# Kernel tuning notes

Hardware: AMD Instinct MI355X
Metric: run time of the kernel (lower is better)

## Reference

```python
import jax, jax.numpy as jnp
import numpy as np

B, N, C = 2, 2048, 1152
H = 16
HD = C // H  # 72
SCALE = HD ** -0.5
NEG = -100000000.0  # -1e8 bias for fp32 masked positions


def setup_inputs() -> dict:
    key = jax.random.key(0)
    k1, k2, k3, k4, k5 = jax.random.split(key, 5)
    x = jax.random.normal(k1, (B, N, C), dtype=jnp.float32)
    attn_mask = jax.random.randint(k2, (B, N), 0, 2, dtype=jnp.int32)
    w_qkv = jax.random.normal(k3, (3 * C, C), dtype=jnp.float32) * 0.02
    w_proj = jax.random.normal(k4, (C, C), dtype=jnp.float32) * 0.02
    b_proj = jax.random.normal(k5, (C,), dtype=jnp.float32) * 0.02
    return {"x": x, "attn_mask": attn_mask, "w_qkv": w_qkv, "w_proj": w_proj, "b_proj": b_proj}


def reference(x, attn_mask, w_qkv, w_proj, b_proj):
    # qkv projection: [B,N,3C] -> [3,B,H,N,HD]
    qkv = (x @ w_qkv.T).reshape(B, N, 3, H, HD).transpose(2, 0, 3, 1, 4)
    q, k, v = qkv[0], qkv[1], qkv[2]

    # additive mask bias from outer product of per-token 0/1 mask
    m = attn_mask.astype(x.dtype)          # [B,N]
    mm = m[:, :, None] * m[:, None, :]      # [B,N,N]
    bias = jnp.where(mm == 0, NEG, jnp.where(mm == 1, 0.0, mm))
    bias = bias[:, None, :, :]              # [B,1,N,N] broadcast over heads

    # math-branch attention: full QK^T, bias add, softmax, NaN patch, AV
    attn = jnp.einsum('bhqd,bhkd->bhqk', q, k) * SCALE + bias
    attn = jax.nn.softmax(attn, axis=-1)
    attn = jnp.where(jnp.isnan(attn), 0.0, attn)
    out = jnp.einsum('bhqk,bhkd->bqhd', attn, v).reshape(B, N, C)

    return out @ w_proj.T + b_proj
```

## Files before the change

kernel.cpp:

```cpp
#include <hip/hip_runtime.h>

#define B_   2
#define N_   2048
#define C_   1152
#define H_   16
#define HD_  72
#define QKV_W 3456
#define SCALE_ 0.11785113019775793f
#define NEG_  -100000000.0f
#define HDP  96
#define HDV  80
#define PRE_  0.1700219068852255f
#define FMAX_ 4.0f
#define KNEG_ 16384.0f

typedef _Float16  f16x8  __attribute__((ext_vector_type(8)));
typedef _Float16  f16x4  __attribute__((ext_vector_type(4)));
typedef float     f32x4  __attribute__((ext_vector_type(4)));

#define GLOAD_LDS16(gp, lp)                                                    \
  __builtin_amdgcn_global_load_lds(                                            \
      (const __attribute__((address_space(1))) void*)(gp),                     \
      (__attribute__((address_space(3))) void*)(lp), 16, 0, 0)

static __device__ __forceinline__ unsigned pack2h(_Float16 a, _Float16 b) {
  union { _Float16 h[2]; unsigned u; } u;
  u.h[0] = a; u.h[1] = b; return u.u;
}
typedef __fp16 fp16v2_builtin __attribute__((ext_vector_type(2)));
static __device__ __forceinline__ unsigned pkrtz(float a, float b) {
  union { fp16v2_builtin h; unsigned u; } u;
  u.h = __builtin_amdgcn_cvt_pkrtz(a, b);
  return u.u;
}

__global__ __launch_bounds__(256)
void split3_f16(const float* __restrict__ x, const float* __restrict__ wq,
                const float* __restrict__ wp,
                _Float16* __restrict__ xf, _Float16* __restrict__ wqf,
                _Float16* __restrict__ wpf,
                _Float16* __restrict__ Qf, _Float16* __restrict__ Kf,
                _Float16* __restrict__ Vt, const int* __restrict__ mask,
                float* __restrict__ meanAcc, int nmv,
                int n8x, int n8q, int n8p) {
  int i = blockIdx.x * 256 + threadIdx.x;
  if (i < nmv) meanAcc[i] = 0.0f;

  const float* src = nullptr; _Float16* dst = nullptr;
  if (i < n8x) { src = x; dst = xf; }
  else {
    i -= n8x;
    if (i < n8q) { src = wq; dst = wqf; }
    else {
      i -= n8q;
      if (i < n8p) { src = wp; dst = wpf; }
      else {
        i -= n8p;
        if (i < 32 * 2048 * 3) {
          const int bh = i / (2048 * 3);
          int rem = i - bh * (2048 * 3);
          const int n = rem / 3, c3 = rem - (rem / 3) * 3;
          f16x8 qp = {}, kp = {};
          if (c3 == 0) {
            qp[0] = (_Float16)1.0f;
            const int kb = (mask[(bh >> 4) * N_ + n] != 0);
            kp[0] = (_Float16)(kb ? -FMAX_ : -KNEG_);
          }
          const size_t base = ((size_t)bh * N_ + n) * HDP + 72 + c3 * 8;
          *(f16x8*)(Qf + base) = qp;
          *(f16x8*)(Kf + base) = kp;
          return;
        }
        i -= 32 * 2048 * 3;
        if (i < 32 * 8 * 256) {
          const int bh = i >> 11, rem = i & 2047;
          const int dp = rem >> 8, nc = rem & 255;
          f16x8 z = {};
          if (dp == 0)
#pragma unroll
            for (int r = 0; r < 8; ++r) z[r] = (_Float16)1.0f;
          *(f16x8*)(Vt + ((size_t)bh * HDV + 72 + dp) * N_ + nc * 8) = z;
        }
        return;
      }
    }
  }

  const float4* p = (const float4*)src + (size_t)i * 2;
  float4 a = p[0], b = p[1];
  float xs[8] = {a.x, a.y, a.z, a.w, b.x, b.y, b.z, b.w};
  f16x8 hv;
#pragma unroll
  for (int r = 0; r < 8; ++r) hv[r] = (_Float16)xs[r];
  *(f16x8*)(dst + (size_t)i * 8) = hv;
}

__global__ __launch_bounds__(256)
void gemm_f16(const _Float16* __restrict__ A, const _Float16* __restrict__ Bm,
              const float* __restrict__ bias, float* __restrict__ Cout,
              int M, int Nn, int K) {
  __shared__ uint4 lds[2][2048];

  const int tid  = threadIdx.x;
  const int wv   = tid >> 6;
  const int lane = tid & 63;
  const int wm   = wv >> 1;
  const int wn   = wv & 1;
  const int bx   = blockIdx.x;
  const int mt   = (bx & 7) * 4 + (bx >> 3);
  const int m0 = mt * 128, n0 = blockIdx.y * 128;

  const char* gp[8];
  int gd[8];
#pragma unroll
  for (int i = 0; i < 8; ++i) {
    const int gid = wv * 8 + i;
    gd[i] = gid * 64;
    if (gid < 16) {
      const int t = gid >> 1, c = gid & 1;
      gp[i] = (const char*)(A + (size_t)(m0 + t * 16 + (lane & 15)) * K +
                            c * 32 + ((lane >> 4) << 3));
    } else {
      const int g2 = gid - 16, t = g2 >> 1, c = g2 & 1;
      gp[i] = (const char*)(Bm + (size_t)(n0 + t * 16 + (lane & 15)) * K +
                            c * 32 + ((lane >> 4) << 3));
    }
  }

#pragma unroll
  for (int i = 0; i < 8; ++i) {
    GLOAD_LDS16(gp[i], &lds[0][gd[i]]);
    gp[i] += 128;
  }

  f32x4 acc[4][4] = {};
  const int nk = K >> 6;

  for (int kt = 0; kt < nk; ++kt) {
    const int cur = kt & 1, nxt = cur ^ 1;
    __syncthreads();

    if (kt < nk - 1) {
#pragma unroll
      for (int i = 0; i < 8; ++i) {
        GLOAD_LDS16(gp[i], &lds[nxt][gd[i]]);
        gp[i] += 128;
      }
    }

    const uint4* cbuf = lds[cur];
#pragma unroll
    for (int c = 0; c < 2; ++c) {
      f16x8 af[4], bf[4];
#pragma unroll
      for (int t = 0; t < 4; ++t) {
        af[t] = *(const f16x8*)&cbuf[(((wm * 4 + t) << 1) | c) * 64 + lane];
        bf[t] = *(const f16x8*)&cbuf[(16 + (((wn * 4 + t) << 1) | c)) * 64 + lane];
      }
#pragma unroll
      for (int i = 0; i < 4; ++i)
#pragma unroll
        for (int j = 0; j < 4; ++j)
          acc[i][j] = __builtin_amdgcn_mfma_f32_16x16x32_f16(af[i], bf[j], acc[i][j], 0, 0, 0);
    }
  }

  const int cl = lane & 15, rq = (lane >> 4) << 2;
#pragma unroll
  for (int j = 0; j < 4; ++j) {
    const int col = n0 + (wn * 4 + j) * 16 + cl;
    const float bv = bias ? bias[col] : 0.0f;
#pragma unroll
    for (int i = 0; i < 4; ++i) {
      const int row = m0 + (wm * 4 + i) * 16 + rq;
#pragma unroll
      for (int r = 0; r < 4; ++r)
        Cout[(size_t)(row + r) * Nn + col] = acc[i][j][r] + bv;
    }
  }
}

__global__ __launch_bounds__(256)
void gemm_qkv_fused(const _Float16* __restrict__ A, const _Float16* __restrict__ Bm,
                    _Float16* __restrict__ Qf, _Float16* __restrict__ Kf,
                    _Float16* __restrict__ Vt, float* __restrict__ meanAcc) {
  __shared__ uint4 lds[2][2048];

  const int K = C_;
  const int tid  = threadIdx.x;
  const int wv   = tid >> 6;
  const int lane = tid & 63;
  const int wm   = wv >> 1;
  const int wn   = wv & 1;
  const int bx   = blockIdx.x;
  const int mt   = (bx & 7) * 4 + (bx >> 3);
  const int m0 = mt * 128, n0 = blockIdx.y * 128;

  const char* gp[8];
  int gd[8];
#pragma unroll
  for (int i = 0; i < 8; ++i) {
    const int gid = wv * 8 + i;
    gd[i] = gid * 64;
    if (gid < 16) {
      const int t = gid >> 1, c = gid & 1;
      gp[i] = (const char*)(A + (size_t)(m0 + t * 16 + (lane & 15)) * K +
                            c * 32 + ((lane >> 4) << 3));
    } else {
      const int g2 = gid - 16, t = g2 >> 1, c = g2 & 1;
      gp[i] = (const char*)(Bm + (size_t)(n0 + t * 16 + (lane & 15)) * K +
                            c * 32 + ((lane >> 4) << 3));
    }
  }

#pragma unroll
  for (int i = 0; i < 8; ++i) {
    GLOAD_LDS16(gp[i], &lds[0][gd[i]]);
    gp[i] += 128;
  }

  f32x4 acc[4][4] = {};
  const int nk = K >> 6;

  for (int kt = 0; kt < nk; ++kt) {
    const int cur = kt & 1, nxt = cur ^ 1;
    __syncthreads();

    if (kt < nk - 1) {
#pragma unroll
      for (int i = 0; i < 8; ++i) {
        GLOAD_LDS16(gp[i], &lds[nxt][gd[i]]);
        gp[i] += 128;
      }
    }

    const uint4* cbuf = lds[cur];
#pragma unroll
    for (int c = 0; c < 2; ++c) {
      f16x8 af[4], bf[4];
#pragma unroll
      for (int t = 0; t < 4; ++t) {
        af[t] = *(const f16x8*)&cbuf[(((wm * 4 + t) << 1) | c) * 64 + lane];
        bf[t] = *(const f16x8*)&cbuf[(16 + (((wn * 4 + t) << 1) | c)) * 64 + lane];
      }
#pragma unroll
      for (int i = 0; i < 4; ++i)
#pragma unroll
        for (int j = 0; j < 4; ++j)
          acc[i][j] = __builtin_amdgcn_mfma_f32_16x16x32_f16(af[i], bf[j], acc[i][j], 0, 0, 0);
    }
  }

  const int s = n0 / C_;
  const int b = m0 >> 11;
  const int nloc = m0 & 2047;
  const int cl = lane & 15, rq = (lane >> 4) << 2;

  if (s < 2) {
    _Float16* dst = (s == 0) ? Qf : Kf;
    const float sc = (s == 0) ? PRE_ : 1.0f;
#pragma unroll
    for (int j = 0; j < 4; ++j) {
      const int col  = n0 + (wn * 4 + j) * 16 + cl;
      const int dseg = col - s * C_;
      const int h = dseg / HD_, hd = dseg - h * HD_;
      _Float16* base =
          dst + ((size_t)(b * H_ + h) * N_ + nloc + wm * 64) * HDP + hd;
#pragma unroll
      for (int i = 0; i < 4; ++i) {
        const int r0 = i * 16 + rq;
#pragma unroll
        for (int r = 0; r < 4; ++r)
          base[(size_t)(r0 + r) * HDP] = (_Float16)(acc[i][j][r] * sc);
      }
    }
  } else {
#pragma unroll
    for (int j = 0; j < 4; ++j) {
      const int col = n0 + (wn * 4 + j) * 16 + cl;
      const int dv  = col - 2 * C_;
      const int h = dv / HD_, hd = dv - h * HD_;
      const int bh = b * H_ + h;
      _Float16* base = Vt + ((size_t)bh * HDV + hd) * N_ + nloc + wm * 64;
      float colsum = 0.0f;
#pragma unroll
      for (int i = 0; i < 4; ++i) {
        const int r0 = i * 16 + rq;
        *(uint2*)(base + r0) =
            make_uint2(pkrtz(acc[i][j][0], acc[i][j][1]),
                       pkrtz(acc[i][j][2], acc[i][j][3]));
        colsum += (acc[i][j][0] + acc[i][j][1]) + (acc[i][j][2] + acc[i][j][3]);
      }
      colsum += __shfl_xor(colsum, 16);
      colsum += __shfl_xor(colsum, 32);
      if ((lane >> 4) == 0)
        atomicAdd(&meanAcc[bh * HD_ + hd], colsum);
    }
  }
}

__global__ __launch_bounds__(256)
void attn_mfma(const _Float16* __restrict__ Qf, const _Float16* __restrict__ Kf,
               const _Float16* __restrict__ Vt, const float* __restrict__ meanV,
               const int* __restrict__ mask, _Float16* __restrict__ att) {
  const int bh = blockIdx.x, qt = blockIdx.y;
  const int b = bh >> 4, h = bh & 15;
  const int tid = threadIdx.x, wv = tid >> 6, lane = tid & 63;
  const int lq = lane & 15;
  const int lg = lane >> 4;
  const int q0 = qt * 128;

  __shared__ uint4 lds[2][22 * 64];
  __shared__ __align__(16) _Float16 Pbuf[2][4][16][72];

  f16x8 qh[2][3];
#pragma unroll
  for (int bd = 0; bd < 2; ++bd) {
    const size_t qoff =
        ((size_t)bh * N_ + q0 + bd * 64 + wv * 16 + lq) * HDP + lg * 8;
#pragma unroll
    for (int c = 0; c < 3; ++c)
      qh[bd][c] = *(const f16x8*)(Qf + qoff + c * 32);
  }

  const _Float16* kb = Kf + (size_t)bh * N_ * HDP;
  const _Float16* vb = Vt + (size_t)bh * HDV * (size_t)N_;

  const int gstart = (wv < 2) ? wv * 6 : 12 + (wv - 2) * 5;
  const int gcount = (wv < 2) ? 6 : 5;
  const char* gptr[6];
  long gstepB[6];
  int gdst[6];
#pragma unroll
  for (int i = 0; i < 6; ++i) {
    int gid = gstart + i;
    if (gid > 21) gid = 21;
    gdst[i] = gid * 64;
    if (gid < 12) {
      const int tile = gid / 3, ch = gid - tile * 3;
      gptr[i] = (const char*)(kb + (size_t)(tile * 16 + lq) * HDP + ch * 32 + lg * 8);
      gstepB[i] = 64 * HDP * 2;
    } else {
      const int v = gid - 12, td = v >> 1, ck = v & 1;
      gptr[i] = (const char*)(vb + (size_t)(td * 16 + lq) * N_ + ck * 32 + lg * 8);
      gstepB[i] = 64 * 2;
    }
  }

#pragma unroll
  for (int i = 0; i < 6; ++i)
    if (i < gcount) {
      GLOAD_LDS16(gptr[i], &lds[0][gdst[i]]);
      gptr[i] += gstepB[i];
    }

  f32x4 Oacc[2][5] = {};

  for (int kt = 0; kt < N_ / 64; ++kt) {
    const int cur = kt & 1, nxt = cur ^ 1;
    __syncthreads();

    if (kt < N_ / 64 - 1) {
#pragma unroll
      for (int i = 0; i < 6; ++i)
        if (i < gcount) {
          GLOAD_LDS16(gptr[i], &lds[nxt][gdst[i]]);
          gptr[i] += gstepB[i];
        }
    }

    const uint4* cbuf = lds[cur];

    f32x4 s[2][4] = {};
#pragma unroll
    for (int ch = 0; ch < 3; ++ch)
#pragma unroll
      for (int t = 0; t < 4; ++t) {
        f16x8 kf = *(const f16x8*)&cbuf[(t * 3 + ch) * 64 + lane];
        s[0][t] = __builtin_amdgcn_mfma_f32_16x16x32_f16(kf, qh[0][ch], s[0][t], 0, 0, 0);
        s[1][t] = __builtin_amdgcn_mfma_f32_16x16x32_f16(kf, qh[1][ch], s[1][t], 0, 0, 0);
      }

#pragma unroll
    for (int bd = 0; bd < 2; ++bd)
#pragma unroll
      for (int t = 0; t < 4; ++t) {
        const float p0 = exp2f(s[bd][t][0]);
        const float p1 = exp2f(s[bd][t][1]);
        const float p2 = exp2f(s[bd][t][2]);
        const float p3 = exp2f(s[bd][t][3]);
        *(uint2*)&Pbuf[bd][wv][lq][t * 16 + 4 * lg] =
            make_uint2(pkrtz(p0, p1), pkrtz(p2, p3));
      }

#pragma unroll
    for (int ck = 0; ck < 2; ++ck) {
      f16x8 pf0 = *(const f16x8*)&Pbuf[0][wv][lq][ck * 32 + lg * 8];
      f16x8 pf1 = *(const f16x8*)&Pbuf[1][wv][lq][ck * 32 + lg * 8];
#pragma unroll
      for (int td = 0; td < 5; ++td) {
        f16x8 vf = *(const f16x8*)&cbuf[(12 + td * 2 + ck) * 64 + lane];
        Oacc[0][td] = __builtin_amdgcn_mfma_f32_16x16x32_f16(vf, pf0, Oacc[0][td], 0, 0, 0);
        Oacc[1][td] = __builtin_amdgcn_mfma_f32_16x16x32_f16(vf, pf1, Oacc[1][td], 0, 0, 0);
      }
    }
  }

  __syncthreads();
  float* osc = (float*)lds;
  float* myo = osc + wv * 16 * 81;
  const int rq = lane >> 2, jj = lane & 3;

#pragma unroll
  for (int bd = 0; bd < 2; ++bd) {
    const float l = __shfl(Oacc[bd][4][0], 32 + lq);
    const float inv = 1.0f / l;
#pragma unroll
    for (int td = 0; td < 5; ++td)
#pragma unroll
      for (int r = 0; r < 4; ++r)
        myo[lq * 81 + td * 16 + 4 * lg + r] = Oacc[bd][td][r] * inv;
    __syncthreads();

    const int q = q0 + bd * 64 + wv * 16 + rq;
    const int qm = (mask[b * N_ + q] != 0);
    const float* rowp = myo + rq * 81 + jj * 18;
    const float* mvp  = meanV + bh * HD_ + jj * 18;
    const size_t obase = ((size_t)(b * N_) + q) * C_ + h * HD_ + jj * 18;
#pragma unroll
    for (int e = 0; e < 9; ++e) {
      const float a = qm ? rowp[2 * e]     : mvp[2 * e]     * (1.0f / 2048.0f);
      const float c = qm ? rowp[2 * e + 1] : mvp[2 * e + 1] * (1.0f / 2048.0f);
      *(unsigned*)(att + obase + 2 * e) = pkrtz(a, c);
    }
    __syncthreads();
  }
}

__global__ __launch_bounds__(256)
void gemm64_nt(const float* __restrict__ A, const float* __restrict__ Bm,
               const float* __restrict__ bias, float* __restrict__ C,
               int M, int N, int K) {
  __shared__ __align__(16) float As[32][68];
  __shared__ __align__(16) float Bs[32][68];
  const int tid = threadIdx.x;
  const int tx = tid & 15, ty = tid >> 4;
  const int m0 = blockIdx.x * 64, n0 = blockIdx.y * 64;
  float acc[4][4] = {};
  for (int k0 = 0; k0 < K; k0 += 32) {
#pragma unroll
    for (int i = 0; i < 2; ++i) {
      const int idx = tid + i * 256;
      const int row = idx >> 3, kc = (idx & 7) << 2;
      float4 a = *(const float4*)(A + (size_t)(m0 + row) * K + k0 + kc);
      As[kc + 0][row] = a.x; As[kc + 1][row] = a.y;
      As[kc + 2][row] = a.z; As[kc + 3][row] = a.w;
      float4 b = *(const float4*)(Bm + (size_t)(n0 + row) * K + k0 + kc);
      Bs[kc + 0][row] = b.x; Bs[kc + 1][row] = b.y;
      Bs[kc + 2][row] = b.z; Bs[kc + 3][row] = b.w;
    }
    __syncthreads();
#pragma unroll
    for (int k = 0; k < 32; ++k) {
      float4 av4 = *(const float4*)&As[k][ty << 2];
      float4 bv4 = *(const float4*)&Bs[k][tx << 2];
      float av[4] = {av4.x, av4.y, av4.z, av4.w};
      float bv[4] = {bv4.x, bv4.y, bv4.z, bv4.w};
#pragma unroll
      for (int i = 0; i < 4; ++i)
#pragma unroll
        for (int j = 0; j < 4; ++j) acc[i][j] += av[i] * bv[j];
    }
    __syncthreads();
  }
#pragma unroll
  for (int i = 0; i < 4; ++i) {
    const int row = m0 + (ty << 2) + i, col = n0 + (tx << 2);
    float4 v = make_float4(acc[i][0], acc[i][1], acc[i][2], acc[i][3]);
    if (bias) {
      v.x += bias[col + 0]; v.y += bias[col + 1];
      v.z += bias[col + 2]; v.w += bias[col + 3];
    }
    *(float4*)(C + (size_t)row * N + col) = v;
  }
}

__global__ __launch_bounds__(256)
void attn_kernel(const float* __restrict__ qkv, const int* __restrict__ mask,
                 float* __restrict__ out) {
  const int qt = blockIdx.x, h = blockIdx.y, b = blockIdx.z;
  const int tid = threadIdx.x;
  const int q0 = qt * 64;
  __shared__ __align__(16) float qT[HD_][68];
  __shared__ __align__(16) float kT[HD_][68];
  __shared__ __align__(16) float vT[HD_][68];
  __shared__ float rowm[64], rowl[64], rowa[64];
  __shared__ float biask[64];
  __shared__ int   mq[64];
  float (*ps)[68] = (float (*)[68])kT;
  const float* qg = qkv + (size_t)(b * N_ + q0) * QKV_W + h * HD_;
  for (int idx = tid; idx < 64 * HD_; idx += 256) {
    const int qi = idx / HD_, d = idx % HD_;
    qT[d][qi] = qg[(size_t)qi * QKV_W + d];
  }
  if (tid < 64) {
    rowm[tid] = -1e30f; rowl[tid] = 0.0f;
    mq[tid] = mask[b * N_ + q0 + tid];
  }
  const int sqg = tid >> 4, skg = tid & 15;
  const int oqg = tid >> 3, ods = tid & 7;
  float o[4][9];
#pragma unroll
  for (int i = 0; i < 4; ++i)
#pragma unroll
    for (int dd = 0; dd < 9; ++dd) o[i][dd] = 0.0f;
  __syncthreads();
  for (int kt = 0; kt < N_ / 64; ++kt) {
    const int k0 = kt * 64;
    const float* kg = qkv + (size_t)(b * N_ + k0) * QKV_W + C_ + h * HD_;
    const float* vg = qkv + (size_t)(b * N_ + k0) * QKV_W + 2 * C_ + h * HD_;
    for (int idx = tid; idx < 64 * HD_; idx += 256) {
      const int kj = idx / HD_, d = idx % HD_;
      kT[d][kj] = kg[(size_t)kj * QKV_W + d];
      vT[d][kj] = vg[(size_t)kj * QKV_W + d];
    }
    if (tid < 64) biask[tid] = (mask[b * N_ + k0 + tid] != 0) ? 0.0f : NEG_;
    __syncthreads();
    float sacc[4][4] = {};
    for (int d = 0; d < HD_; ++d) {
      float4 qv4 = *(const float4*)&qT[d][sqg << 2];
      float4 kv4 = *(const float4*)&kT[d][skg << 2];
      float qa[4] = {qv4.x, qv4.y, qv4.z, qv4.w};
      float ka[4] = {kv4.x, kv4.y, kv4.z, kv4.w};
#pragma unroll
      for (int i = 0; i < 4; ++i)
#pragma unroll
        for (int j = 0; j < 4; ++j) sacc[i][j] += qa[i] * ka[j];
    }
    __syncthreads();
#pragma unroll
    for (int i = 0; i < 4; ++i) {
      const int qi = (sqg << 2) + i;
      const int qm2 = mq[qi];
#pragma unroll
      for (int j = 0; j < 4; ++j) {
        const int kj = (skg << 2) + j;
        const float bias = (qm2 != 0) ? biask[kj] : NEG_;
        ps[qi][kj] = sacc[i][j] * SCALE_ + bias;
      }
    }
    __syncthreads();
    if (tid < 64) {
      float mt = -1e30f;
#pragma unroll
      for (int j4 = 0; j4 < 16; ++j4) {
        float4 p4 = *(const float4*)&ps[tid][j4 << 2];
        mt = fmaxf(mt, fmaxf(fmaxf(p4.x, p4.y), fmaxf(p4.z, p4.w)));
      }
      const float mo = rowm[tid];
      const float nm = fmaxf(mo, mt);
      const float a = __expf(mo - nm);
      float sum = 0.0f;
#pragma unroll
      for (int j4 = 0; j4 < 16; ++j4) {
        float4 p4 = *(const float4*)&ps[tid][j4 << 2];
        p4.x = __expf(p4.x - nm); p4.y = __expf(p4.y - nm);
        p4.z = __expf(p4.z - nm); p4.w = __expf(p4.w - nm);
        sum += p4.x + p4.y + p4.z + p4.w;
        *(float4*)&ps[tid][j4 << 2] = p4;
      }
      rowl[tid] = rowl[tid] * a + sum;
      rowm[tid] = nm;
      rowa[tid] = a;
    }
    __syncthreads();
    if (tid < 128) {
#pragma unroll
      for (int i = 0; i < 4; ++i) {
        const float a = rowa[(oqg << 2) + i];
#pragma unroll
        for (int dd = 0; dd < 9; ++dd) o[i][dd] *= a;
      }
      for (int k4 = 0; k4 < 16; ++k4) {
        float4 pv4[4];
#pragma unroll
        for (int i = 0; i < 4; ++i)
          pv4[i] = *(const float4*)&ps[(oqg << 2) + i][k4 << 2];
        float pa[4][4];
#pragma unroll
        for (int i = 0; i < 4; ++i) {
          pa[i][0] = pv4[i].x; pa[i][1] = pv4[i].y;
          pa[i][2] = pv4[i].z; pa[i][3] = pv4[i].w;
        }
#pragma unroll
        for (int dd = 0; dd < 9; ++dd) {
          float4 vv4 = *(const float4*)&vT[ods * 9 + dd][k4 << 2];
          float va[4] = {vv4.x, vv4.y, vv4.z, vv4.w};
#pragma unroll
          for (int i = 0; i < 4; ++i)
            o[i][dd] += pa[i][0] * va[0] + pa[i][1] * va[1] +
                        pa[i][2] * va[2] + pa[i][3] * va[3];
        }
      }
    }
    __syncthreads();
  }
  if (tid < 128) {
#pragma unroll
    for (int i = 0; i < 4; ++i) {
      const int qi = (oqg << 2) + i;
      const float inv = 1.0f / rowl[qi];
      const size_t base = (size_t)(b * N_ + q0 + qi) * C_ + h * HD_ + ods * 9;
#pragma unroll
      for (int dd = 0; dd < 9; ++dd) out[base + dd] = o[i][dd] * inv;
    }
  }
}

extern "C" void kernel_launch(void* const* d_in, const int* in_sizes, int n_in,
                              void* d_out, int out_size, void* d_ws, size_t ws_size,
                              hipStream_t stream) {
  (void)in_sizes; (void)n_in; (void)out_size;

  const float* x      = (const float*)d_in[0];
  const int*   mask   = (const int*)  d_in[1];
  const float* w_qkv  = (const float*)d_in[2];
  const float* w_proj = (const float*)d_in[3];
  const float* b_proj = (const float*)d_in[4];
  float* out = (float*)d_out;

  const size_t XE = (size_t)B_ * N_ * C_;
  const size_t WQ = (size_t)QKV_W * C_;
  const size_t WP = (size_t)C_ * C_;
  const size_t QKVE = (size_t)B_ * N_ * QKV_W;
  const size_t QKE  = (size_t)B_ * H_ * N_ * HDP;
  const size_t VTE  = (size_t)B_ * H_ * HDV * N_;
  const int    MVN  = B_ * H_ * HD_;

  char* w = (char*)d_ws;
  _Float16* att  = (_Float16*)w;
  _Float16* x_f  = att + XE;
  _Float16* wq_f = x_f + XE;
  _Float16* wp_f = wq_f + WQ;
  _Float16* Qf   = wp_f + WP;
  _Float16* Kf   = Qf + QKE;
  _Float16* Vt   = Kf + QKE;
  float* meanAcc = (float*)(Vt + VTE);
  const size_t need = (size_t)((char*)(meanAcc + MVN) - w);

  if (ws_size >= need) {
    const int n8x = (int)(XE / 8), n8q = (int)(WQ / 8), n8p = (int)(WP / 8);
    const int npadQK = 32 * 2048 * 3;
    const int npadV  = 32 * 8 * 256;
    const int total  = n8x + n8q + n8p + npadQK + npadV;
    split3_f16<<<(total + 255) / 256, 256, 0, stream>>>(
        x, w_qkv, w_proj, x_f, wq_f, wp_f, Qf, Kf, Vt, mask,
        meanAcc, MVN, n8x, n8q, n8p);

    gemm_qkv_fused<<<dim3(32, 27), 256, 0, stream>>>(x_f, wq_f, Qf, Kf, Vt,
                                                     meanAcc);

    attn_mfma<<<dim3(32, 16), 256, 0, stream>>>(Qf, Kf, Vt, meanAcc, mask, att);

    gemm_f16<<<dim3(32, 9), 256, 0, stream>>>(att, wp_f, b_proj, out,
                                              B_ * N_, C_, C_);
  } else {
    float* qkv_f = (float*)d_ws;
    float* att_f = qkv_f + QKVE;
    gemm64_nt<<<dim3(64, 54), 256, 0, stream>>>(x, w_qkv, nullptr, qkv_f,
                                                B_ * N_, QKV_W, C_);
    attn_kernel<<<dim3(32, 16, 2), 256, 0, stream>>>(qkv_f, mask, att_f);
    gemm64_nt<<<dim3(64, 18), 256, 0, stream>>>(att_f, w_proj, b_proj, out,
                                                B_ * N_, C_, C_);
  }
}
```

Measured before the change: 273.0 us.

## Double query rows per attention block and cache K fragments in registers

Each attention block now covers 256 query rows (four 64-row groups) instead of 128, so every K/V tile staged in LDS is reused across twice as many queries and the grid shrinks from 512 to 256 blocks. The K fragments for a tile are loaded from LDS into registers once and reused for all four query groups, and launch bounds are set to one block per CU to give the compiler more registers. The cost is higher register and LDS pressure and only 256 blocks, about one per CU on MI355X (256 CUs), which cuts occupancy and latency hiding.

```diff
diff --git a/kernel.cpp b/kernel.cpp
--- a/kernel.cpp
+++ b/kernel.cpp
@@ -299,7 +299,7 @@
   }
 }
 
-__global__ __launch_bounds__(256)
+__global__ __launch_bounds__(256, 1)
 void attn_mfma(const _Float16* __restrict__ Qf, const _Float16* __restrict__ Kf,
                const _Float16* __restrict__ Vt, const float* __restrict__ meanV,
                const int* __restrict__ mask, _Float16* __restrict__ att) {
@@ -308,14 +308,14 @@
   const int tid = threadIdx.x, wv = tid >> 6, lane = tid & 63;
   const int lq = lane & 15;
   const int lg = lane >> 4;
-  const int q0 = qt * 128;
+  const int q0 = qt * 256;
 
   __shared__ uint4 lds[2][22 * 64];
-  __shared__ __align__(16) _Float16 Pbuf[2][4][16][72];
-
-  f16x8 qh[2][3];
-#pragma unroll
-  for (int bd = 0; bd < 2; ++bd) {
+  __shared__ __align__(16) _Float16 Pbuf[4][4][16][72];
+
+  f16x8 qh[4][3];
+#pragma unroll
+  for (int bd = 0; bd < 4; ++bd) {
     const size_t qoff =
         ((size_t)bh * N_ + q0 + bd * 64 + wv * 16 + lq) * HDP + lg * 8;
 #pragma unroll
@@ -354,7 +354,7 @@
       gptr[i] += gstepB[i];
     }
 
-  f32x4 Oacc[2][5] = {};
+  f32x4 Oacc[4][5] = {};
 
   for (int kt = 0; kt < N_ / 64; ++kt) {
     const int cur = kt & 1, nxt = cur ^ 1;
@@ -371,37 +371,44 @@
 
     const uint4* cbuf = lds[cur];
 
-    f32x4 s[2][4] = {};
-#pragma unroll
-    for (int ch = 0; ch < 3; ++ch)
+    f16x8 kfr[12];
+#pragma unroll
+    for (int g = 0; g < 12; ++g)
+      kfr[g] = *(const f16x8*)&cbuf[g * 64 + lane];
+
+#pragma unroll
+    for (int bd = 0; bd < 4; ++bd) {
+      f32x4 s[4] = {};
+#pragma unroll
+      for (int ch = 0; ch < 3; ++ch)
+#pragma unroll
+        for (int t = 0; t < 4; ++t)
+          s[t] = __builtin_amdgcn_mfma_f32_16x16x32_f16(kfr[t * 3 + ch],
+                                                        qh[bd][ch], s[t], 0, 0, 0);
 #pragma unroll
       for (int t = 0; t < 4; ++t) {
-        f16x8 kf = *(const f16x8*)&cbuf[(t * 3 + ch) * 64 + lane];
-        s[0][t] = __builtin_amdgcn_mfma_f32_16x16x32_f16(kf, qh[0][ch], s[0][t], 0, 0, 0);
-        s[1][t] = __builtin_amdgcn_mfma_f32_16x16x32_f16(kf, qh[1][ch], s[1][t], 0, 0, 0);
-      }
-
-#pragma unroll
-    for (int bd = 0; bd < 2; ++bd)
-#pragma unroll
-      for (int t = 0; t < 4; ++t) {
-        const float p0 = exp2f(s[bd][t][0]);
-        const float p1 = exp2f(s[bd][t][1]);
-        const float p2 = exp2f(s[bd][t][2]);
-        const float p3 = exp2f(s[bd][t][3]);
+        const float p0 = exp2f(s[t][0]);
+        const float p1 = exp2f(s[t][1]);
+        const float p2 = exp2f(s[t][2]);
+        const float p3 = exp2f(s[t][3]);
         *(uint2*)&Pbuf[bd][wv][lq][t * 16 + 4 * lg] =
             make_uint2(pkrtz(p0, p1), pkrtz(p2, p3));
       }
+    }
 
 #pragma unroll
     for (int ck = 0; ck < 2; ++ck) {
-      f16x8 pf0 = *(const f16x8*)&Pbuf[0][wv][lq][ck * 32 + lg * 8];
-      f16x8 pf1 = *(const f16x8*)&Pbuf[1][wv][lq][ck * 32 + lg * 8];
+      f16x8 pf[4];
+#pragma unroll
+      for (int bd = 0; bd < 4; ++bd)
+        pf[bd] = *(const f16x8*)&Pbuf[bd][wv][lq][ck * 32 + lg * 8];
 #pragma unroll
       for (int td = 0; td < 5; ++td) {
         f16x8 vf = *(const f16x8*)&cbuf[(12 + td * 2 + ck) * 64 + lane];
-        Oacc[0][td] = __builtin_amdgcn_mfma_f32_16x16x32_f16(vf, pf0, Oacc[0][td], 0, 0, 0);
-        Oacc[1][td] = __builtin_amdgcn_mfma_f32_16x16x32_f16(vf, pf1, Oacc[1][td], 0, 0, 0);
+#pragma unroll
+        for (int bd = 0; bd < 4; ++bd)
+          Oacc[bd][td] = __builtin_amdgcn_mfma_f32_16x16x32_f16(vf, pf[bd],
+                                                                Oacc[bd][td], 0, 0, 0);
       }
     }
   }
@@ -412,7 +419,7 @@
   const int rq = lane >> 2, jj = lane & 3;
 
 #pragma unroll
-  for (int bd = 0; bd < 2; ++bd) {
+  for (int bd = 0; bd < 4; ++bd) {
     const float l = __shfl(Oacc[bd][4][0], 32 + lq);
     const float inv = 1.0f / l;
 #pragma unroll
@@ -660,7 +667,7 @@
     gemm_qkv_fused<<<dim3(32, 27), 256, 0, stream>>>(x_f, wq_f, Qf, Kf, Vt,
                                                      meanAcc);
 
-    attn_mfma<<<dim3(32, 16), 256, 0, stream>>>(Qf, Kf, Vt, meanAcc, mask, att);
+    attn_mfma<<<dim3(32, 8), 256, 0, stream>>>(Qf, Kf, Vt, meanAcc, mask, att);
 
     gemm_f16<<<dim3(32, 9), 256, 0, stream>>>(att, wp_f, b_proj, out,
                                               B_ * N_, C_, C_);
```

Result: slower. 296.7 us (+8.7%).
